# Optimization experiments

Measured on AMD Instinct MI355X. Metric: run time of the kernel, lower is better.

The kernel has to match this reference:

```python
import jax, jax.numpy as jnp
import numpy as np

CAPACITY_FACTOR = 0.67
AUX_LOSS_COEF = 0.001


def setup_inputs() -> dict:
    key = jax.random.key(0)
    k1, k2 = jax.random.split(key)
    B, S, D = 4, 4096, 2048
    x = jax.random.normal(k1, (B, S, D), dtype=jnp.float32)
    # all-True mask -> static number of active tokens (jit-friendly, same math)
    current_mask = jnp.ones((B, S), dtype=bool)
    w_router = jax.random.normal(k2, (1, D), dtype=jnp.float32) / np.sqrt(D)
    return {"x": x, "current_mask": current_mask, "w_router": w_router}


def reference(x, current_mask, w_router):
    B, S, D = x.shape
    N = B * S
    flat = x.reshape(N, D)
    # router: Linear(d_model, 1, bias=False) then sigmoid -> per-token score
    scores = jax.nn.sigmoid(flat @ w_router[0])  # [N]
    # exclude inactive tokens from selection (mask all-True here, so no-op)
    masked_scores = jnp.where(current_mask.reshape(N), scores, -jnp.inf)
    num_active = N  # static: mask is all-True by construction
    num_to_keep = max(1, int(num_active * CAPACITY_FACTOR))
    top_scores, top_idx = jax.lax.top_k(masked_scores, num_to_keep)
    # scatter selected flat positions into a fresh boolean mask
    new_mask = jnp.zeros(N, dtype=bool).at[top_idx].set(True).reshape(B, S)
    aux_loss = -jnp.mean(top_scores) * AUX_LOSS_COEF
    return new_mask, aux_loss
```

## Files before the change

### kernel.cpp

```cpp
#include <hip/hip_runtime.h>
#include <hip/hip_bf16.h>


#define D_MODEL 2048
#define NSEL_THREADS 1024
#define CHUNK 16

__global__ __launch_bounds__(256) void score_kernel(const float* __restrict__ x,
                                                    const float* __restrict__ w,
                                                    float* __restrict__ scores,
                                                    int n_tok) {
    const int wave = threadIdx.x >> 6;
    const int lane = threadIdx.x & 63;
    const int tok  = blockIdx.x * 4 + wave;
    if (tok >= n_tok) return;

    const float4* xr = (const float4*)(x + (size_t)tok * D_MODEL);
    const float4* wr = (const float4*)w;

    double acc = 0.0;
#pragma unroll
    for (int i = 0; i < D_MODEL / 256; ++i) {
        float4 xv = xr[i * 64 + lane];
        float4 wv = wr[i * 64 + lane];
        acc += (double)xv.x * (double)wv.x + (double)xv.y * (double)wv.y
             + (double)xv.z * (double)wv.z + (double)xv.w * (double)wv.w;
    }
    for (int off = 32; off > 0; off >>= 1)
        acc += __shfl_down(acc, off, 64);

    if (lane == 0) {
        float logit = (float)acc;
        scores[tok] = 1.0f / (1.0f + expf(-logit));
    }
}

__global__ __launch_bounds__(NSEL_THREADS) void select_kernel(const float* __restrict__ scores,
                                                              float* __restrict__ out,
                                                              int n, int k) {
    __shared__ unsigned int whist[16 * 257];
    __shared__ int wsum[16];
    __shared__ unsigned int sel_prefix_sh;
    __shared__ int sel_remaining_sh;
    __shared__ int warp_part[16];
    __shared__ double sum_sh[16];

    const int tid = threadIdx.x;
    const int wv  = tid >> 6;
    const int ln  = tid & 63;
    const int beg = tid * CHUNK;

    unsigned int key[CHUNK];
    {
        const uint4* sv = (const uint4*)(scores + beg);
#pragma unroll
        for (int q = 0; q < CHUNK / 4; ++q) {
            uint4 v = sv[q];
            key[q * 4 + 0] = v.x; key[q * 4 + 1] = v.y;
            key[q * 4 + 2] = v.z; key[q * 4 + 3] = v.w;
        }
    }

    unsigned int prefix = 0;
    unsigned int pmask  = 0;
    int remaining = k;

#pragma unroll
    for (int pass = 0; pass < 4; ++pass) {
        const int shift = 24 - pass * 8;
        for (int i = tid; i < 16 * 257; i += NSEL_THREADS) whist[i] = 0;
        __syncthreads();

        if (pass == 0) {
#pragma unroll
            for (int j = 0; j < CHUNK; ++j) {
                unsigned int dig = key[j] >> 24;
                unsigned long long pending = ~0ull;
                while (pending) {
                    int lead = __ffsll((unsigned long long)pending) - 1;
                    unsigned int d0 = __shfl((int)dig, lead, 64);
                    unsigned long long match = __ballot(dig == d0) & pending;
                    if (ln == lead)
                        atomicAdd(&whist[wv * 257 + d0], (unsigned int)__popcll(match));
                    pending &= ~match;
                }
            }
        } else {
#pragma unroll
            for (int j = 0; j < CHUNK; ++j)
                if ((key[j] & pmask) == prefix)
                    atomicAdd(&whist[wv * 257 + ((key[j] >> shift) & 255u)], 1u);
        }
        __syncthreads();

        int c = 0;
        if (tid < 256) {
#pragma unroll
            for (int w = 0; w < 16; ++w) c += (int)whist[w * 257 + tid];
        }
        int sc = c;
        for (int off = 1; off < 64; off <<= 1) {
            int v = __shfl_down(sc, off, 64);
            if (ln + off < 64) sc += v;
        }
        if (tid < 256 && ln == 0) wsum[wv] = sc;
        __syncthreads();
        if (tid < 256) {
            int hi = 0;
            for (int w = wv + 1; w < 4; ++w) hi += wsum[w];
            const int S_excl = hi + (sc - c);
            if (S_excl < remaining && remaining <= S_excl + c) {
                sel_prefix_sh    = prefix | ((unsigned int)tid << shift);
                sel_remaining_sh = remaining - S_excl;
            }
        }
        __syncthreads();
        prefix    = sel_prefix_sh;
        remaining = sel_remaining_sh;
        pmask    |= (0xFFu << shift);
        __syncthreads();
    }
    const unsigned int tkey = prefix;
    const int ties_needed   = remaining;

    double lsum = 0.0;
#pragma unroll
    for (int j = 0; j < CHUNK; ++j)
        if (key[j] > tkey) lsum += (double)__uint_as_float(key[j]);
    for (int off = 32; off > 0; off >>= 1)
        lsum += __shfl_down(lsum, off, 64);
    if (ln == 0) sum_sh[wv] = lsum;

    int lties = 0;
#pragma unroll
    for (int j = 0; j < CHUNK; ++j)
        if (key[j] == tkey) ++lties;

    int sc2 = lties;
    for (int off = 1; off < 64; off <<= 1) {
        int v = __shfl_up(sc2, off, 64);
        if (ln >= off) sc2 += v;
    }
    if (ln == 63) warp_part[wv] = sc2;
    __syncthreads();
    if (wv == 0 && ln < 16) {
        int v = warp_part[ln];
        for (int off = 1; off < 16; off <<= 1) {
            int u = __shfl_up(v, off, 64);
            if (ln >= off) v += u;
        }
        warp_part[ln] = v;
    }
    __syncthreads();
    const int wave_off = (wv == 0) ? 0 : warp_part[wv - 1];
    const int excl = wave_off + sc2 - lties;

    float mv[CHUNK];
    int taken = 0;
#pragma unroll
    for (int j = 0; j < CHUNK; ++j) {
        if (key[j] > tkey) {
            mv[j] = 1.0f;
        } else if (key[j] == tkey) {
            mv[j] = (excl + taken < ties_needed) ? 1.0f : 0.0f;
            ++taken;
        } else {
            mv[j] = 0.0f;
        }
    }
    {
        float4* ov = (float4*)(out + beg);
#pragma unroll
        for (int q = 0; q < CHUNK / 4; ++q)
            ov[q] = make_float4(mv[q * 4 + 0], mv[q * 4 + 1],
                                mv[q * 4 + 2], mv[q * 4 + 3]);
    }

    if (tid == 0) {
        double s = 0.0;
        for (int i = 0; i < 16; ++i) s += sum_sh[i];
        s += (double)ties_needed * (double)__uint_as_float(tkey);
        out[n] = (float)(-(s / (double)k) * 0.001);
    }
}

extern "C" void kernel_launch(void* const* d_in, const int* in_sizes, int n_in,
                              void* d_out, int out_size, void* d_ws, size_t ws_size,
                              hipStream_t stream) {
    const float* x = (const float*)d_in[0];
    const float* w = (const float*)d_in[2];

    const int d = in_sizes[2];
    const int n = in_sizes[0] / d;

    float* scores = (float*)d_ws;
    float* out    = (float*)d_out;

    int k = (int)((double)n * 0.67);
    if (k < 1) k = 1;

    score_kernel<<<(n + 3) / 4, 256, 0, stream>>>(x, w, scores, n);
    select_kernel<<<1, NSEL_THREADS, 0, stream>>>(scores, out, n, k);
}
```

Measured before the change: 206.4 us.

## Fuse score and select kernels using a last-block ticket counter

Merges the router scoring kernel and the single-block top-k selection kernel into one launch. Each 1024-thread block scores 16 tokens, then increments a global ticket, and the last block to finish performs the radix-select over all scores. This removes a kernel launch and the gap between kernels, but adds a memset launch and runs the scoring phase in large blocks, which may lower occupancy for the bandwidth-bound dot products.

```diff
diff --git a/kernel.cpp b/kernel.cpp
--- a/kernel.cpp
+++ b/kernel.cpp
@@ -6,48 +6,53 @@
 #define NSEL_THREADS 1024
 #define CHUNK 16
 
-__global__ __launch_bounds__(256) void score_kernel(const float* __restrict__ x,
-                                                    const float* __restrict__ w,
-                                                    float* __restrict__ scores,
-                                                    int n_tok) {
-    const int wave = threadIdx.x >> 6;
-    const int lane = threadIdx.x & 63;
-    const int tok  = blockIdx.x * 4 + wave;
-    if (tok >= n_tok) return;
-
-    const float4* xr = (const float4*)(x + (size_t)tok * D_MODEL);
-    const float4* wr = (const float4*)w;
-
-    double acc = 0.0;
-#pragma unroll
-    for (int i = 0; i < D_MODEL / 256; ++i) {
-        float4 xv = xr[i * 64 + lane];
-        float4 wv = wr[i * 64 + lane];
-        acc += (double)xv.x * (double)wv.x + (double)xv.y * (double)wv.y
-             + (double)xv.z * (double)wv.z + (double)xv.w * (double)wv.w;
-    }
-    for (int off = 32; off > 0; off >>= 1)
-        acc += __shfl_down(acc, off, 64);
-
-    if (lane == 0) {
-        float logit = (float)acc;
-        scores[tok] = 1.0f / (1.0f + expf(-logit));
-    }
-}
-
-__global__ __launch_bounds__(NSEL_THREADS) void select_kernel(const float* __restrict__ scores,
-                                                              float* __restrict__ out,
-                                                              int n, int k) {
+__global__ __launch_bounds__(NSEL_THREADS) void router_fused_kernel(
+        const float* __restrict__ x,
+        const float* __restrict__ w,
+        float* __restrict__ scores,
+        unsigned int* __restrict__ ticket_ctr,
+        float* __restrict__ out,
+        int n, int k) {
     __shared__ unsigned int whist[16 * 257];
     __shared__ int wsum[16];
     __shared__ unsigned int sel_prefix_sh;
     __shared__ int sel_remaining_sh;
     __shared__ int warp_part[16];
     __shared__ double sum_sh[16];
+    __shared__ unsigned int ticket_sh;
 
     const int tid = threadIdx.x;
     const int wv  = tid >> 6;
     const int ln  = tid & 63;
+
+    {
+        const int tok = blockIdx.x * 16 + wv;
+        const float4* xr = (const float4*)(x + (size_t)tok * D_MODEL);
+        const float4* wr = (const float4*)w;
+
+        double acc = 0.0;
+#pragma unroll
+        for (int i = 0; i < D_MODEL / 256; ++i) {
+            float4 xv = xr[i * 64 + ln];
+            float4 wv4 = wr[i * 64 + ln];
+            acc += (double)xv.x * (double)wv4.x + (double)xv.y * (double)wv4.y
+                 + (double)xv.z * (double)wv4.z + (double)xv.w * (double)wv4.w;
+        }
+        for (int off = 32; off > 0; off >>= 1)
+            acc += __shfl_down(acc, off, 64);
+        if (ln == 0) {
+            float logit = (float)acc;
+            scores[tok] = 1.0f / (1.0f + expf(-logit));
+        }
+    }
+
+    __syncthreads();
+    __threadfence();
+    if (tid == 0) ticket_sh = atomicAdd(ticket_ctr, 1u);
+    __syncthreads();
+    if (ticket_sh != (unsigned int)(gridDim.x - 1)) return;
+    __threadfence();
+
     const int beg = tid * CHUNK;
 
     unsigned int key[CHUNK];
@@ -96,7 +101,7 @@
         int c = 0;
         if (tid < 256) {
 #pragma unroll
-            for (int w = 0; w < 16; ++w) c += (int)whist[w * 257 + tid];
+            for (int w2 = 0; w2 < 16; ++w2) c += (int)whist[w2 * 257 + tid];
         }
         int sc = c;
         for (int off = 1; off < 64; off <<= 1) {
@@ -107,7 +112,7 @@
         __syncthreads();
         if (tid < 256) {
             int hi = 0;
-            for (int w = wv + 1; w < 4; ++w) hi += wsum[w];
+            for (int w2 = wv + 1; w2 < 4; ++w2) hi += wsum[w2];
             const int S_excl = hi + (sc - c);
             if (S_excl < remaining && remaining <= S_excl + c) {
                 sel_prefix_sh    = prefix | ((unsigned int)tid << shift);
@@ -194,11 +199,13 @@
     const int n = in_sizes[0] / d;
 
     float* scores = (float*)d_ws;
-    float* out    = (float*)d_out;
+    unsigned int* ticket = (unsigned int*)((char*)d_ws + (size_t)n * 4);
+    float* out = (float*)d_out;
 
     int k = (int)((double)n * 0.67);
     if (k < 1) k = 1;
 
-    score_kernel<<<(n + 3) / 4, 256, 0, stream>>>(x, w, scores, n);
-    select_kernel<<<1, NSEL_THREADS, 0, stream>>>(scores, out, n, k);
+    (void)hipMemsetAsync(ticket, 0, 4, stream);
+    router_fused_kernel<<<n / 16, NSEL_THREADS, 0, stream>>>(
+        x, w, scores, ticket, out, n, k);
 }
```

Result: slower. 449.7 us (+117.9%).
